# Performance work log

Hardware: AMD Instinct MI355X
Metric: run time of the kernel (lower is better)

Reference implementation:

```python
import jax, jax.numpy as jnp
import numpy as np

N = 100_000      # nodes
E = 1_600_000    # edges (avg degree 16)
DN = 64          # node feature dim
DE = 64          # edge feature dim


def _w(k, shape):
    fan_in = shape[0]
    return jax.random.normal(k, shape, dtype=jnp.float32) / np.sqrt(fan_in)


def setup_inputs() -> dict:
    key = jax.random.key(0)
    ks = jax.random.split(key, 12)
    x = jax.random.normal(ks[0], (N, DN), dtype=jnp.float32)
    e = jax.random.normal(ks[1], (E, DE), dtype=jnp.float32)
    senders = jax.random.randint(ks[2], (E,), 0, N)
    receivers = jax.random.randint(ks[3], (E,), 0, N)
    return {
        "x": x, "e": e, "senders": senders, "receivers": receivers,
        "We1": _w(ks[4], (DE + 2 * DN, DE)), "be1": jnp.zeros((DE,), jnp.float32),
        "We2": _w(ks[5], (DE, DE)),          "be2": jnp.zeros((DE,), jnp.float32),
        "We3": _w(ks[6], (DE, DE)),          "be3": jnp.zeros((DE,), jnp.float32),
        "Wn1": _w(ks[7], (DN + DE, DN)),     "bn1": jnp.zeros((DN,), jnp.float32),
        "Wn2": _w(ks[8], (DN, DN)),          "bn2": jnp.zeros((DN,), jnp.float32),
        "Wn3": _w(ks[9], (DN, DN)),          "bn3": jnp.zeros((DN,), jnp.float32),
    }


def reference(x, e, senders, receivers,
              We1, be1, We2, be2, We3, be3,
              Wn1, bn1, Wn2, bn2, Wn3, bn3):
    # --- EdgeBlock: concat(edge, sender, receiver) -> MLP ---
    h = jnp.concatenate([e, x[senders], x[receivers]], axis=-1)  # [E, DE+2*DN]
    h = jax.nn.relu(h @ We1 + be1)
    h = jax.nn.relu(h @ We2 + be2)
    e_new = h @ We3 + be3                                        # [E, DE]
    # --- NodeBlock: sum-aggregate receiving edges, concat(node, agg) -> MLP ---
    agg = jax.ops.segment_sum(e_new, receivers, num_segments=N)  # [N, DE]
    g = jnp.concatenate([x, agg], axis=-1)                       # [N, DN+DE]
    g = jax.nn.relu(g @ Wn1 + bn1)
    g = jax.nn.relu(g @ Wn2 + bn2)
    x_new = g @ Wn3 + bn3                                        # [N, DN]
    return x_new
```

## Files before the change

kernel.cpp:

```cpp
#include <hip/hip_runtime.h>

#define NN 100000
#define NE 1600000
#define NT (NE / 16)

typedef short v8s __attribute__((ext_vector_type(8)));
typedef float v4f __attribute__((ext_vector_type(4)));
typedef unsigned short v4u16 __attribute__((ext_vector_type(4)));

__device__ __forceinline__ unsigned short f2bf(float f) {
    union { float f; unsigned int u; } v; v.f = f;
    unsigned int r = v.u + 0x7FFFu + ((v.u >> 16) & 1u);
    return (unsigned short)(r >> 16);
}

__device__ __forceinline__ v8s pack8(float4 a, float4 b) {
    union { v8s v; unsigned short u[8]; } t;
    t.u[0] = f2bf(a.x); t.u[1] = f2bf(a.y); t.u[2] = f2bf(a.z); t.u[3] = f2bf(a.w);
    t.u[4] = f2bf(b.x); t.u[5] = f2bf(b.y); t.u[6] = f2bf(b.z); t.u[7] = f2bf(b.w);
    return t.v;
}

__device__ __forceinline__ int wfrag(int row, int k) {
    return row * 32 + ((((k >> 3) & 3) ^ ((row >> 1) & 3)) << 3) + (k & 7);
}
__device__ __forceinline__ int hoff(int m, int k) {
    return (k >> 5) * 512 + m * 32 + ((((k >> 3) & 3) ^ ((m >> 1) & 3)) << 3) + (k & 7);
}

__device__ __forceinline__ void store_bf4(unsigned short* base, int row, int k, float4 v) {
    v4u16 p;
    p.x = f2bf(v.x); p.y = f2bf(v.y); p.z = f2bf(v.z); p.w = f2bf(v.w);
    *(v4u16*)(base + ((k >> 5) * 2048 + row * 32 + (k & 31))) = p;
}

#define MFMA16(acc, a, b) acc = __builtin_amdgcn_mfma_f32_16x16x32_bf16(a, b, acc, 0, 0, 0)

__global__ __launch_bounds__(512, 4) void edge_kernel(
    const float* __restrict__ x, const float* __restrict__ e,
    const int* __restrict__ snd, const int* __restrict__ rcv,
    const float* __restrict__ We1, const float* __restrict__ be1,
    const float* __restrict__ We2, const float* __restrict__ be2,
    const float* __restrict__ We3, const float* __restrict__ be3,
    float* agg)
{
    extern __shared__ unsigned short smem[];
    unsigned short* WT1 = smem;
    unsigned short* WT2 = WT1 + 12288;
    unsigned short* WT3 = WT2 + 4096;
    unsigned short* HS  = WT3 + 4096;

    const int tid = threadIdx.x;

    for (int idx = tid; idx < 192 * 64; idx += 512) {
        int k = idx >> 6, n = idx & 63;
        WT1[(k >> 5) * 2048 + wfrag(n, k & 31)] = f2bf(We1[idx]);
    }
    for (int idx = tid; idx < 64 * 64; idx += 512) {
        int k = idx >> 6, n = idx & 63;
        int off = (k >> 5) * 2048 + wfrag(n, k & 31);
        WT2[off] = f2bf(We2[idx]);
        WT3[off] = f2bf(We3[idx]);
    }

    const int lane = tid & 63;
    const int wv   = tid >> 6;
    const int l15  = lane & 15;
    const int quad = lane >> 4;
    unsigned short* H = HS + wv * 1024;

    float b1v[4], b2v[4], b3v[4];
#pragma unroll
    for (int nt = 0; nt < 4; ++nt) {
        b1v[nt] = be1[nt * 16 + l15];
        b2v[nt] = be2[nt * 16 + l15];
        b3v[nt] = be3[nt * 16 + l15];
    }

    const int swz = l15 * 32 + ((quad ^ ((l15 >> 1) & 3)) << 3);

    __syncthreads();

    const int nwaves = gridDim.x * (blockDim.x >> 6);
    int wt = blockIdx.x * (blockDim.x >> 6) + wv;

    int er = wt * 16 + l15;
    int s0 = snd[er], r0 = rcv[er];

    while (wt < NT) {
        const int ebase = wt * 16;
        const int s = s0, rcur = r0;

        const float* erow = e + (size_t)(ebase + l15) * 64 + quad * 8;
        const float* xs   = x + (size_t)s    * 64 + quad * 8;
        const float* xr   = x + (size_t)rcur * 64 + quad * 8;

        float4 e00 = *(const float4*)(erow);
        float4 e01 = *(const float4*)(erow + 4);
        float4 e10 = *(const float4*)(erow + 32);
        float4 e11 = *(const float4*)(erow + 36);
        float4 s00 = *(const float4*)(xs);
        float4 s01 = *(const float4*)(xs + 4);
        float4 s10 = *(const float4*)(xs + 32);
        float4 s11 = *(const float4*)(xs + 36);
        float4 r00 = *(const float4*)(xr);
        float4 r01 = *(const float4*)(xr + 4);
        float4 r10 = *(const float4*)(xr + 32);
        float4 r11 = *(const float4*)(xr + 36);

        const int wtn = wt + nwaves;
        if (wtn < NT) {
            int ern = wtn * 16 + l15;
            s0 = snd[ern];
            r0 = rcv[ern];
        }

        v8s af[6];
        af[0] = pack8(e00, e01); af[1] = pack8(e10, e11);
        af[2] = pack8(s00, s01); af[3] = pack8(s10, s11);
        af[4] = pack8(r00, r01); af[5] = pack8(r10, r11);

        {
            v4f acc[4];
#pragma unroll
            for (int nt = 0; nt < 4; ++nt) acc[nt] = (v4f){0.f, 0.f, 0.f, 0.f};
#pragma unroll
            for (int kb = 0; kb < 6; ++kb) {
#pragma unroll
                for (int nt = 0; nt < 4; ++nt) {
                    v8s bf = *(const v8s*)(WT1 + kb * 2048 + nt * 512 + swz);
                    MFMA16(acc[nt], af[kb], bf);
                }
            }
#pragma unroll
            for (int nt = 0; nt < 4; ++nt) {
                int kk = nt * 16 + l15;
#pragma unroll
                for (int r = 0; r < 4; ++r) {
                    float v = acc[nt][r] + b1v[nt];
                    v = v > 0.f ? v : 0.f;
                    H[hoff(quad * 4 + r, kk)] = f2bf(v);
                }
            }
        }

        {
            v8s a0 = *(const v8s*)(H + swz);
            v8s a1 = *(const v8s*)(H + 512 + swz);
            v4f acc[4];
#pragma unroll
            for (int nt = 0; nt < 4; ++nt) acc[nt] = (v4f){0.f, 0.f, 0.f, 0.f};
#pragma unroll
            for (int nt = 0; nt < 4; ++nt) {
                v8s bf0 = *(const v8s*)(WT2 + nt * 512 + swz);
                MFMA16(acc[nt], a0, bf0);
                v8s bf1 = *(const v8s*)(WT2 + 2048 + nt * 512 + swz);
                MFMA16(acc[nt], a1, bf1);
            }
#pragma unroll
            for (int nt = 0; nt < 4; ++nt) {
                int kk = nt * 16 + l15;
#pragma unroll
                for (int r = 0; r < 4; ++r) {
                    float v = acc[nt][r] + b2v[nt];
                    v = v > 0.f ? v : 0.f;
                    H[hoff(quad * 4 + r, kk)] = f2bf(v);
                }
            }
        }

        {
            v8s a0 = *(const v8s*)(H + swz);
            v8s a1 = *(const v8s*)(H + 512 + swz);
            v4f acc[4];
#pragma unroll
            for (int nt = 0; nt < 4; ++nt) acc[nt] = (v4f){0.f, 0.f, 0.f, 0.f};
#pragma unroll
            for (int nt = 0; nt < 4; ++nt) {
                v8s bf0 = *(const v8s*)(WT3 + nt * 512 + swz);
                MFMA16(acc[nt], a0, bf0);
                v8s bf1 = *(const v8s*)(WT3 + 2048 + nt * 512 + swz);
                MFMA16(acc[nt], a1, bf1);
            }
#pragma unroll
            for (int ri = 0; ri < 4; ++ri) {
                int dst = __shfl(rcur, quad * 4 + ri, 16);
                float* aggrow = agg + (size_t)dst * 64;
#pragma unroll
                for (int nt = 0; nt < 4; ++nt) {
                    unsafeAtomicAdd(aggrow + nt * 16 + l15, acc[nt][ri] + b3v[nt]);
                }
            }
        }

        wt = wtn;
    }
}

__global__ __launch_bounds__(256, 2) void node_kernel(
    const float* __restrict__ x,
    const float* __restrict__ Wn1, const float* __restrict__ bn1,
    const float* __restrict__ Wn2, const float* __restrict__ bn2,
    const float* __restrict__ Wn3, const float* __restrict__ bn3,
    float* aggout)
{
    extern __shared__ unsigned short smem[];
    unsigned short* WT1 = smem;
    unsigned short* WT2 = WT1 + 8192;
    unsigned short* WT3 = WT2 + 4096;
    unsigned short* A   = WT3 + 4096;

    const int tid = threadIdx.x;

    for (int idx = tid; idx < 128 * 64; idx += 256) {
        int k = idx >> 6, n = idx & 63;
        WT1[(k >> 5) * 2048 + n * 32 + (k & 31)] = f2bf(Wn1[idx]);
    }
    for (int idx = tid; idx < 64 * 64; idx += 256) {
        int k = idx >> 6, n = idx & 63;
        int off = (k >> 5) * 2048 + n * 32 + (k & 31);
        WT2[off] = f2bf(Wn2[idx]);
        WT3[off] = f2bf(Wn3[idx]);
    }

    const int lane = tid & 63;
    const int wv   = tid >> 6;
    const int l15  = lane & 15;
    const int quad = lane >> 4;
    const int astrip = wv * 16;

    float b1v[4], b2v[4], b3v[4];
#pragma unroll
    for (int nt = 0; nt < 4; ++nt) {
        b1v[nt] = bn1[nt * 16 + l15];
        b2v[nt] = bn2[nt * 16 + l15];
        b3v[nt] = bn3[nt * 16 + l15];
    }

    const int arow = (astrip + l15) * 32 + quad * 8;
    const int brow = l15 * 32 + quad * 8;
    const int nbase = blockIdx.x * 64;

    __syncthreads();

#pragma unroll
    for (int t = 0; t < 4; ++t) {
        int idx = tid + t * 256;
        int row = idx >> 4;
        int k0  = (idx & 15) * 4;
        int node = nbase + row;
        float4 vx = {0.f, 0.f, 0.f, 0.f}, va = {0.f, 0.f, 0.f, 0.f};
        if (node < NN) {
            vx = *(const float4*)(x + (size_t)node * 64 + k0);
            va = *(const float4*)(aggout + (size_t)node * 64 + k0);
        }
        store_bf4(A, row, k0, vx);
        store_bf4(A, row, 64 + k0, va);
    }
    __syncthreads();

    {
        v4f acc[4];
#pragma unroll
        for (int nt = 0; nt < 4; ++nt) acc[nt] = (v4f){0.f, 0.f, 0.f, 0.f};
#pragma unroll
        for (int kb = 0; kb < 4; ++kb) {
            v8s af = *(const v8s*)(A + kb * 2048 + arow);
#pragma unroll
            for (int nt = 0; nt < 4; ++nt) {
                v8s bf = *(const v8s*)(WT1 + kb * 2048 + brow + nt * 512);
                MFMA16(acc[nt], af, bf);
            }
        }
#pragma unroll
        for (int nt = 0; nt < 4; ++nt) {
            int kk = nt * 16 + l15;
#pragma unroll
            for (int r = 0; r < 4; ++r) {
                int m = astrip + quad * 4 + r;
                float v = acc[nt][r] + b1v[nt];
                v = v > 0.f ? v : 0.f;
                A[(kk >> 5) * 2048 + m * 32 + (kk & 31)] = f2bf(v);
            }
        }
    }

    {
        v4f acc[4];
#pragma unroll
        for (int nt = 0; nt < 4; ++nt) acc[nt] = (v4f){0.f, 0.f, 0.f, 0.f};
#pragma unroll
        for (int kb = 0; kb < 2; ++kb) {
            v8s af = *(const v8s*)(A + kb * 2048 + arow);
#pragma unroll
            for (int nt = 0; nt < 4; ++nt) {
                v8s bf = *(const v8s*)(WT2 + kb * 2048 + brow + nt * 512);
                MFMA16(acc[nt], af, bf);
            }
        }
#pragma unroll
        for (int nt = 0; nt < 4; ++nt) {
            int kk = nt * 16 + l15;
#pragma unroll
            for (int r = 0; r < 4; ++r) {
                int m = astrip + quad * 4 + r;
                float v = acc[nt][r] + b2v[nt];
                v = v > 0.f ? v : 0.f;
                A[(2 + (kk >> 5)) * 2048 + m * 32 + (kk & 31)] = f2bf(v);
            }
        }
    }

    {
        v4f acc[4];
#pragma unroll
        for (int nt = 0; nt < 4; ++nt) acc[nt] = (v4f){0.f, 0.f, 0.f, 0.f};
#pragma unroll
        for (int kb = 0; kb < 2; ++kb) {
            v8s af = *(const v8s*)(A + (2 + kb) * 2048 + arow);
#pragma unroll
            for (int nt = 0; nt < 4; ++nt) {
                v8s bf = *(const v8s*)(WT3 + kb * 2048 + brow + nt * 512);
                MFMA16(acc[nt], af, bf);
            }
        }
#pragma unroll
        for (int r = 0; r < 4; ++r) {
            int node = nbase + astrip + quad * 4 + r;
            if (node < NN) {
#pragma unroll
                for (int nt = 0; nt < 4; ++nt) {
                    aggout[(size_t)node * 64 + nt * 16 + l15] = acc[nt][r] + b3v[nt];
                }
            }
        }
    }
}

extern "C" void kernel_launch(void* const* d_in, const int* in_sizes, int n_in,
                              void* d_out, int out_size, void* d_ws, size_t ws_size,
                              hipStream_t stream) {
    const float* x   = (const float*)d_in[0];
    const float* e   = (const float*)d_in[1];
    const int*   snd = (const int*)d_in[2];
    const int*   rcv = (const int*)d_in[3];
    const float* We1 = (const float*)d_in[4];  const float* be1 = (const float*)d_in[5];
    const float* We2 = (const float*)d_in[6];  const float* be2 = (const float*)d_in[7];
    const float* We3 = (const float*)d_in[8];  const float* be3 = (const float*)d_in[9];
    const float* Wn1 = (const float*)d_in[10]; const float* bn1 = (const float*)d_in[11];
    const float* Wn2 = (const float*)d_in[12]; const float* bn2 = (const float*)d_in[13];
    const float* Wn3 = (const float*)d_in[14]; const float* bn3 = (const float*)d_in[15];
    float* out = (float*)d_out;

    hipMemsetAsync(out, 0, (size_t)NN * 64 * sizeof(float), stream);

    edge_kernel<<<512, 512, 57344, stream>>>(x, e, snd, rcv,
                                             We1, be1, We2, be2, We3, be3,
                                             out);

    node_kernel<<<(NN + 63) / 64, 256, 49152, stream>>>(x,
                                                        Wn1, bn1, Wn2, bn2, Wn3, bn3,
                                                        out);
}
```

Measured before the change: 854.7 us.

## Replace float atomic scatter with CSR bucketing and segmented gather reduction

Builds a receiver histogram and exclusive scan on the device, so each edge's bf16 output row is written into a CSR-ordered slot claimed with one integer atomic per edge. The node kernel then sums each node's incoming edge rows itself, replacing 64 float atomics per edge into the aggregate buffer. The trade-off is a 200MB bf16 intermediate write and read, plus extra histogram and scan launches, one of them a single-block serial scan. Accumulation order becomes nondeterministic and edge outputs are rounded to bf16 before summation. The old atomic path is kept as a fallback when the workspace is too small.

```diff
diff --git a/kernel.cpp b/kernel.cpp
--- a/kernel.cpp
+++ b/kernel.cpp
@@ -12,6 +12,10 @@
     union { float f; unsigned int u; } v; v.f = f;
     unsigned int r = v.u + 0x7FFFu + ((v.u >> 16) & 1u);
     return (unsigned short)(r >> 16);
+}
+__device__ __forceinline__ float bf2f(unsigned short u) {
+    union { unsigned int i; float f; } v; v.i = ((unsigned int)u) << 16;
+    return v.f;
 }
 
 __device__ __forceinline__ v8s pack8(float4 a, float4 b) {
@@ -36,7 +40,393 @@
 
 #define MFMA16(acc, a, b) acc = __builtin_amdgcn_mfma_f32_16x16x32_bf16(a, b, acc, 0, 0, 0)
 
-__global__ __launch_bounds__(512, 4) void edge_kernel(
+__global__ void hist_kernel(const int* __restrict__ rcv, int* __restrict__ cursor) {
+    int i = blockIdx.x * blockDim.x + threadIdx.x;
+    int stride = gridDim.x * blockDim.x;
+    for (; i < NE; i += stride) atomicAdd(&cursor[rcv[i]], 1);
+}
+
+__global__ __launch_bounds__(1024) void scan_kernel(int* __restrict__ cursor,
+                                                    int* __restrict__ rowptr) {
+    __shared__ int wsum[16];
+    __shared__ int chunk_total;
+    const int tid = threadIdx.x;
+    const int lane = tid & 63, wv = tid >> 6;
+    int running = 0;
+    for (int base = 0; base < NN; base += 1024) {
+        int i = base + tid;
+        int v = (i < NN) ? cursor[i] : 0;
+        int s = v;
+#pragma unroll
+        for (int d = 1; d < 64; d <<= 1) {
+            int t = __shfl_up(s, d);
+            if (lane >= d) s += t;
+        }
+        if (lane == 63) wsum[wv] = s;
+        __syncthreads();
+        if (wv == 0 && lane < 16) {
+            int ws = wsum[lane];
+            int ss = ws;
+#pragma unroll
+            for (int d = 1; d < 16; d <<= 1) {
+                int t = __shfl_up(ss, d, 16);
+                if (lane >= d) ss += t;
+            }
+            wsum[lane] = ss - ws;
+        }
+        __syncthreads();
+        int excl = running + wsum[wv] + (s - v);
+        if (i < NN) { rowptr[i] = excl; cursor[i] = excl; }
+        if (tid == 1023) chunk_total = wsum[15] + s;
+        __syncthreads();
+        running += chunk_total;
+        __syncthreads();
+    }
+    if (tid == 0) rowptr[NN] = running;
+}
+
+__global__ __launch_bounds__(512, 4) void edge_kernel_csr(
+    const float* __restrict__ x, const float* __restrict__ e,
+    const int* __restrict__ snd, const int* __restrict__ rcv,
+    const float* __restrict__ We1, const float* __restrict__ be1,
+    const float* __restrict__ We2, const float* __restrict__ be2,
+    const float* __restrict__ We3, const float* __restrict__ be3,
+    unsigned short* __restrict__ enew, int* __restrict__ cursor)
+{
+    extern __shared__ unsigned short smem[];
+    unsigned short* WT1 = smem;
+    unsigned short* WT2 = WT1 + 12288;
+    unsigned short* WT3 = WT2 + 4096;
+    unsigned short* HS  = WT3 + 4096;
+
+    const int tid = threadIdx.x;
+
+    for (int idx = tid; idx < 192 * 64; idx += 512) {
+        int k = idx >> 6, n = idx & 63;
+        WT1[(k >> 5) * 2048 + wfrag(n, k & 31)] = f2bf(We1[idx]);
+    }
+    for (int idx = tid; idx < 64 * 64; idx += 512) {
+        int k = idx >> 6, n = idx & 63;
+        int off = (k >> 5) * 2048 + wfrag(n, k & 31);
+        WT2[off] = f2bf(We2[idx]);
+        WT3[off] = f2bf(We3[idx]);
+    }
+
+    const int lane = tid & 63;
+    const int wv   = tid >> 6;
+    const int l15  = lane & 15;
+    const int quad = lane >> 4;
+    unsigned short* H = HS + wv * 1024;
+
+    float b1v[4], b2v[4], b3v[4];
+#pragma unroll
+    for (int nt = 0; nt < 4; ++nt) {
+        b1v[nt] = be1[nt * 16 + l15];
+        b2v[nt] = be2[nt * 16 + l15];
+        b3v[nt] = be3[nt * 16 + l15];
+    }
+
+    const int swz = l15 * 32 + ((quad ^ ((l15 >> 1) & 3)) << 3);
+
+    __syncthreads();
+
+    const int nwaves = gridDim.x * (blockDim.x >> 6);
+    int wt = blockIdx.x * (blockDim.x >> 6) + wv;
+
+    int er = wt * 16 + l15;
+    int s0 = snd[er], r0 = rcv[er];
+
+    const int crow = lane >> 2, cchk = lane & 3;
+
+    while (wt < NT) {
+        const int ebase = wt * 16;
+        const int s = s0, rcur = r0;
+
+        const float* erow = e + (size_t)(ebase + l15) * 64 + quad * 8;
+        const float* xs   = x + (size_t)s    * 64 + quad * 8;
+        const float* xr   = x + (size_t)rcur * 64 + quad * 8;
+
+        float4 e00 = *(const float4*)(erow);
+        float4 e01 = *(const float4*)(erow + 4);
+        float4 e10 = *(const float4*)(erow + 32);
+        float4 e11 = *(const float4*)(erow + 36);
+        float4 s00 = *(const float4*)(xs);
+        float4 s01 = *(const float4*)(xs + 4);
+        float4 s10 = *(const float4*)(xs + 32);
+        float4 s11 = *(const float4*)(xs + 36);
+        float4 r00 = *(const float4*)(xr);
+        float4 r01 = *(const float4*)(xr + 4);
+        float4 r10 = *(const float4*)(xr + 32);
+        float4 r11 = *(const float4*)(xr + 36);
+
+        const int wtn = wt + nwaves;
+        if (wtn < NT) {
+            int ern = wtn * 16 + l15;
+            s0 = snd[ern];
+            r0 = rcv[ern];
+        }
+
+        v8s af[6];
+        af[0] = pack8(e00, e01); af[1] = pack8(e10, e11);
+        af[2] = pack8(s00, s01); af[3] = pack8(s10, s11);
+        af[4] = pack8(r00, r01); af[5] = pack8(r10, r11);
+
+        {
+            v4f acc[4];
+#pragma unroll
+            for (int nt = 0; nt < 4; ++nt) acc[nt] = (v4f){0.f, 0.f, 0.f, 0.f};
+#pragma unroll
+            for (int kb = 0; kb < 6; ++kb) {
+#pragma unroll
+                for (int nt = 0; nt < 4; ++nt) {
+                    v8s bf = *(const v8s*)(WT1 + kb * 2048 + nt * 512 + swz);
+                    MFMA16(acc[nt], af[kb], bf);
+                }
+            }
+#pragma unroll
+            for (int nt = 0; nt < 4; ++nt) {
+                int kk = nt * 16 + l15;
+#pragma unroll
+                for (int r = 0; r < 4; ++r) {
+                    float v = acc[nt][r] + b1v[nt];
+                    v = v > 0.f ? v : 0.f;
+                    H[hoff(quad * 4 + r, kk)] = f2bf(v);
+                }
+            }
+        }
+
+        {
+            v8s a0 = *(const v8s*)(H + swz);
+            v8s a1 = *(const v8s*)(H + 512 + swz);
+            v4f acc[4];
+#pragma unroll
+            for (int nt = 0; nt < 4; ++nt) acc[nt] = (v4f){0.f, 0.f, 0.f, 0.f};
+#pragma unroll
+            for (int nt = 0; nt < 4; ++nt) {
+                v8s bf0 = *(const v8s*)(WT2 + nt * 512 + swz);
+                MFMA16(acc[nt], a0, bf0);
+                v8s bf1 = *(const v8s*)(WT2 + 2048 + nt * 512 + swz);
+                MFMA16(acc[nt], a1, bf1);
+            }
+#pragma unroll
+            for (int nt = 0; nt < 4; ++nt) {
+                int kk = nt * 16 + l15;
+#pragma unroll
+                for (int r = 0; r < 4; ++r) {
+                    float v = acc[nt][r] + b2v[nt];
+                    v = v > 0.f ? v : 0.f;
+                    H[hoff(quad * 4 + r, kk)] = f2bf(v);
+                }
+            }
+        }
+
+        {
+            v8s a0 = *(const v8s*)(H + swz);
+            v8s a1 = *(const v8s*)(H + 512 + swz);
+            v4f acc[4];
+#pragma unroll
+            for (int nt = 0; nt < 4; ++nt) acc[nt] = (v4f){0.f, 0.f, 0.f, 0.f};
+#pragma unroll
+            for (int nt = 0; nt < 4; ++nt) {
+                v8s bf0 = *(const v8s*)(WT3 + nt * 512 + swz);
+                MFMA16(acc[nt], a0, bf0);
+                v8s bf1 = *(const v8s*)(WT3 + 2048 + nt * 512 + swz);
+                MFMA16(acc[nt], a1, bf1);
+            }
+#pragma unroll
+            for (int nt = 0; nt < 4; ++nt) {
+                int kk = nt * 16 + l15;
+#pragma unroll
+                for (int r = 0; r < 4; ++r) {
+                    H[hoff(quad * 4 + r, kk)] = f2bf(acc[nt][r] + b3v[nt]);
+                }
+            }
+            int pos = 0;
+            if (quad == 0) pos = atomicAdd(cursor + rcur, 1);
+            int posr = __shfl(pos, crow);
+            unsigned short* dst = enew + (size_t)posr * 64 + cchk * 8;
+#pragma unroll
+            for (int kb = 0; kb < 2; ++kb) {
+                v8s d = *(const v8s*)(H + kb * 512 + crow * 32 +
+                                      ((cchk ^ ((crow >> 1) & 3)) << 3));
+                *(v8s*)(dst + kb * 32) = d;
+            }
+        }
+
+        wt = wtn;
+    }
+}
+
+__global__ __launch_bounds__(256, 2) void node_kernel_csr(
+    const float* __restrict__ x,
+    const unsigned short* __restrict__ enew, const int* __restrict__ rowptr,
+    const float* __restrict__ Wn1, const float* __restrict__ bn1,
+    const float* __restrict__ Wn2, const float* __restrict__ bn2,
+    const float* __restrict__ Wn3, const float* __restrict__ bn3,
+    float* __restrict__ out)
+{
+    extern __shared__ unsigned short smem[];
+    unsigned short* WT1 = smem;
+    unsigned short* WT2 = WT1 + 8192;
+    unsigned short* WT3 = WT2 + 4096;
+    unsigned short* A   = WT3 + 4096;
+
+    const int tid = threadIdx.x;
+
+    for (int idx = tid; idx < 128 * 64; idx += 256) {
+        int k = idx >> 6, n = idx & 63;
+        WT1[(k >> 5) * 2048 + n * 32 + (k & 31)] = f2bf(Wn1[idx]);
+    }
+    for (int idx = tid; idx < 64 * 64; idx += 256) {
+        int k = idx >> 6, n = idx & 63;
+        int off = (k >> 5) * 2048 + n * 32 + (k & 31);
+        WT2[off] = f2bf(Wn2[idx]);
+        WT3[off] = f2bf(Wn3[idx]);
+    }
+
+    const int lane = tid & 63;
+    const int wv   = tid >> 6;
+    const int l15  = lane & 15;
+    const int quad = lane >> 4;
+    const int astrip = wv * 16;
+    const int nbase = blockIdx.x * 64;
+
+    float b1v[4], b2v[4], b3v[4];
+#pragma unroll
+    for (int nt = 0; nt < 4; ++nt) {
+        b1v[nt] = bn1[nt * 16 + l15];
+        b2v[nt] = bn2[nt * 16 + l15];
+        b3v[nt] = bn3[nt * 16 + l15];
+    }
+
+#pragma unroll
+    for (int t = 0; t < 2; ++t) {
+        int idx = tid + t * 256;
+        int row = idx >> 3;
+        int k0  = (idx & 7) * 8;
+        int node = nbase + row;
+        float4 v0 = {0.f, 0.f, 0.f, 0.f}, v1 = {0.f, 0.f, 0.f, 0.f};
+        if (node < NN) {
+            v0 = *(const float4*)(x + (size_t)node * 64 + k0);
+            v1 = *(const float4*)(x + (size_t)node * 64 + k0 + 4);
+        }
+        store_bf4(A, row, k0, v0);
+        store_bf4(A, row, k0 + 4, v1);
+    }
+
+    const int rsub = lane >> 3;
+    const int csub = lane & 7;
+    for (int j = 0; j < 16; ++j) {
+        int node = nbase + astrip + j;
+        float av[8] = {0.f, 0.f, 0.f, 0.f, 0.f, 0.f, 0.f, 0.f};
+        if (node < NN) {
+            int start = rowptr[node], end = rowptr[node + 1];
+            for (int r0 = start; r0 < end; r0 += 8) {
+                int rr = r0 + rsub;
+                if (rr < end) {
+                    v8s d = *(const v8s*)(enew + (size_t)rr * 64 + csub * 8);
+#pragma unroll
+                    for (int k = 0; k < 8; ++k) av[k] += bf2f((unsigned short)d[k]);
+                }
+            }
+        }
+#pragma unroll
+        for (int m = 8; m < 64; m <<= 1) {
+#pragma unroll
+            for (int k = 0; k < 8; ++k) av[k] += __shfl_xor(av[k], m);
+        }
+        if (rsub == 0) {
+            float4 a = {av[0], av[1], av[2], av[3]};
+            float4 b = {av[4], av[5], av[6], av[7]};
+            store_bf4(A, astrip + j, 64 + csub * 8, a);
+            store_bf4(A, astrip + j, 64 + csub * 8 + 4, b);
+        }
+    }
+
+    const int arow = (astrip + l15) * 32 + quad * 8;
+    const int brow = l15 * 32 + quad * 8;
+
+    __syncthreads();
+
+    {
+        v4f acc[4];
+#pragma unroll
+        for (int nt = 0; nt < 4; ++nt) acc[nt] = (v4f){0.f, 0.f, 0.f, 0.f};
+#pragma unroll
+        for (int kb = 0; kb < 4; ++kb) {
+            v8s af = *(const v8s*)(A + kb * 2048 + arow);
+#pragma unroll
+            for (int nt = 0; nt < 4; ++nt) {
+                v8s bf = *(const v8s*)(WT1 + kb * 2048 + brow + nt * 512);
+                MFMA16(acc[nt], af, bf);
+            }
+        }
+#pragma unroll
+        for (int nt = 0; nt < 4; ++nt) {
+            int kk = nt * 16 + l15;
+#pragma unroll
+            for (int r = 0; r < 4; ++r) {
+                int m = astrip + quad * 4 + r;
+                float v = acc[nt][r] + b1v[nt];
+                v = v > 0.f ? v : 0.f;
+                A[(kk >> 5) * 2048 + m * 32 + (kk & 31)] = f2bf(v);
+            }
+        }
+    }
+
+    {
+        v4f acc[4];
+#pragma unroll
+        for (int nt = 0; nt < 4; ++nt) acc[nt] = (v4f){0.f, 0.f, 0.f, 0.f};
+#pragma unroll
+        for (int kb = 0; kb < 2; ++kb) {
+            v8s af = *(const v8s*)(A + kb * 2048 + arow);
+#pragma unroll
+            for (int nt = 0; nt < 4; ++nt) {
+                v8s bf = *(const v8s*)(WT2 + kb * 2048 + brow + nt * 512);
+                MFMA16(acc[nt], af, bf);
+            }
+        }
+#pragma unroll
+        for (int nt = 0; nt < 4; ++nt) {
+            int kk = nt * 16 + l15;
+#pragma unroll
+            for (int r = 0; r < 4; ++r) {
+                int m = astrip + quad * 4 + r;
+                float v = acc[nt][r] + b2v[nt];
+                v = v > 0.f ? v : 0.f;
+                A[(2 + (kk >> 5)) * 2048 + m * 32 + (kk & 31)] = f2bf(v);
+            }
+        }
+    }
+
+    {
+        v4f acc[4];
+#pragma unroll
+        for (int nt = 0; nt < 4; ++nt) acc[nt] = (v4f){0.f, 0.f, 0.f, 0.f};
+#pragma unroll
+        for (int kb = 0; kb < 2; ++kb) {
+            v8s af = *(const v8s*)(A + (2 + kb) * 2048 + arow);
+#pragma unroll
+            for (int nt = 0; nt < 4; ++nt) {
+                v8s bf = *(const v8s*)(WT3 + kb * 2048 + brow + nt * 512);
+                MFMA16(acc[nt], af, bf);
+            }
+        }
+#pragma unroll
+        for (int r = 0; r < 4; ++r) {
+            int node = nbase + astrip + quad * 4 + r;
+            if (node < NN) {
+#pragma unroll
+                for (int nt = 0; nt < 4; ++nt) {
+                    out[(size_t)node * 64 + nt * 16 + l15] = acc[nt][r] + b3v[nt];
+                }
+            }
+        }
+    }
+}
+
+__global__ __launch_bounds__(512, 4) void edge_kernel_atomic(
     const float* __restrict__ x, const float* __restrict__ e,
     const int* __restrict__ snd, const int* __restrict__ rcv,
     const float* __restrict__ We1, const float* __restrict__ be1,
@@ -197,7 +587,7 @@
     }
 }
 
-__global__ __launch_bounds__(256, 2) void node_kernel(
+__global__ __launch_bounds__(256, 2) void node_kernel_atomic(
     const float* __restrict__ x,
     const float* __restrict__ Wn1, const float* __restrict__ bn1,
     const float* __restrict__ Wn2, const float* __restrict__ bn2,
@@ -352,13 +742,32 @@
     const float* Wn3 = (const float*)d_in[14]; const float* bn3 = (const float*)d_in[15];
     float* out = (float*)d_out;
 
-    hipMemsetAsync(out, 0, (size_t)NN * 64 * sizeof(float), stream);
-
-    edge_kernel<<<512, 512, 57344, stream>>>(x, e, snd, rcv,
-                                             We1, be1, We2, be2, We3, be3,
-                                             out);
-
-    node_kernel<<<(NN + 63) / 64, 256, 49152, stream>>>(x,
-                                                        Wn1, bn1, Wn2, bn2, Wn3, bn3,
+    const size_t ENEW_BYTES = (size_t)NE * 64 * 2;
+    const size_t ROWPTR_OFF = ENEW_BYTES;
+    const size_t CURSOR_OFF = ROWPTR_OFF + 400016;
+    const size_t WS_REQ     = CURSOR_OFF + (size_t)NN * 4;
+
+    if (d_ws != nullptr && ws_size >= WS_REQ) {
+        unsigned short* enew = (unsigned short*)d_ws;
+        int* rowptr = (int*)((char*)d_ws + ROWPTR_OFF);
+        int* cursor = (int*)((char*)d_ws + CURSOR_OFF);
+
+        hipMemsetAsync(cursor, 0, (size_t)NN * 4, stream);
+        hist_kernel<<<1024, 256, 0, stream>>>(rcv, cursor);
+        scan_kernel<<<1, 1024, 0, stream>>>(cursor, rowptr);
+        edge_kernel_csr<<<512, 512, 57344, stream>>>(x, e, snd, rcv,
+                                                     We1, be1, We2, be2, We3, be3,
+                                                     enew, cursor);
+        node_kernel_csr<<<(NN + 63) / 64, 256, 49152, stream>>>(x, enew, rowptr,
+                                                                Wn1, bn1, Wn2, bn2, Wn3, bn3,
+                                                                out);
+    } else {
+        hipMemsetAsync(out, 0, (size_t)NN * 64 * sizeof(float), stream);
+        edge_kernel_atomic<<<512, 512, 57344, stream>>>(x, e, snd, rcv,
+                                                        We1, be1, We2, be2, We3, be3,
                                                         out);
-}
+        node_kernel_atomic<<<(NN + 63) / 64, 256, 49152, stream>>>(x,
+                                                                   Wn1, bn1, Wn2, bn2, Wn3, bn3,
+                                                                   out);
+    }
+}
```

Measured after the change: 996.8 us. +16.6%, slower.
